# Kernel tuning notes

Measured on AMD Instinct MI355X. Metric: run time of the kernel, lower is better.

The kernel has to match this reference:

```python
import jax, jax.numpy as jnp
import numpy as np

N_NODES, N_EDGES, N_FEAT = 50000, 500000, 128
HID, LAT, N_GRAPHS = 256, 64, 512
HEADS, DH = 8, 32  # GAT: 8 heads x 32 = 256
EPS = 1e-5


def _seg_softmax(logits, seg, num):
    m = jax.ops.segment_max(logits, seg, num_segments=num)
    m = jnp.where(jnp.isfinite(m), m, 0.0)
    e = jnp.exp(logits - m[seg])
    s = jax.ops.segment_sum(e, seg, num_segments=num)
    return e / jnp.maximum(s[seg], 1e-16)


def _bn(h, g, b):  # BatchNorm1d, batch statistics
    mu = h.mean(0)
    var = h.var(0)
    return (h - mu) * jax.lax.rsqrt(var + EPS) * g + b


def _ln(h, g, b):
    mu = h.mean(-1, keepdims=True)
    var = h.var(-1, keepdims=True)
    return (h - mu) * jax.lax.rsqrt(var + EPS) * g + b


def setup_inputs() -> dict:
    key = jax.random.key(0)
    ks = iter(jax.random.split(key, 40))
    f = lambda *s: jax.random.normal(next(ks), s, dtype=jnp.float32) * 0.05
    inp = {
        'x': jax.random.normal(next(ks), (N_NODES, N_FEAT), dtype=jnp.float32),
        'W_emb': f(N_FEAT, HID), 'b_emb': f(HID),
        'W_gcn': f(HID, HID), 'b_gcn': f(HID),
        'W_gat': f(HID, HID), 'a_src': f(HEADS, DH), 'a_dst': f(HEADS, DH), 'b_gat': f(HID),
        'W_l': f(HID, HID), 'b_l': f(HID), 'W_r': f(HID, HID),
        'bn_gamma': jnp.ones((3, HID), jnp.float32), 'bn_beta': jnp.zeros((3, HID), jnp.float32),
        'Wg1': f(HID, HID // 2), 'bg1': f(HID // 2), 'Wg2': f(HID // 2, 1), 'bg2': f(1),
        'Wm1': f(HID, HID), 'bm1': f(HID), 'ln_m_g': jnp.ones(HID, jnp.float32), 'ln_m_b': jnp.zeros(HID, jnp.float32),
        'Wm2': f(HID, LAT), 'bm2': f(LAT),
        'Wv1': f(HID, HID), 'bv1': f(HID), 'ln_v_g': jnp.ones(HID, jnp.float32), 'ln_v_b': jnp.zeros(HID, jnp.float32),
        'Wv2': f(HID, LAT), 'bv2': f(LAT),
        'edge_index': jax.random.randint(next(ks), (2, N_EDGES), 0, N_NODES, dtype=jnp.int64),
        'batch': jnp.sort(jax.random.randint(next(ks), (N_NODES,), 0, N_GRAPHS, dtype=jnp.int64)),
    }
    return inp


def _forward(x, W_emb, b_emb, W_gcn, b_gcn, W_gat, a_src, a_dst, b_gat,
             W_l, b_l, W_r, bn_gamma, bn_beta, Wg1, bg1, Wg2, bg2,
             Wm1, bm1, ln_m_g, ln_m_b, Wm2, bm2, Wv1, bv1, ln_v_g, ln_v_b, Wv2, bv2,
             edge_index, batch):
    N = x.shape[0]
    loops = jnp.arange(N)
    src_sl = jnp.concatenate([edge_index[0], loops])  # with self-loops (GCN/GAT)
    dst_sl = jnp.concatenate([edge_index[1], loops])

    h = x @ W_emb + b_emb  # [N, HID]

    # --- layer 0: GCNConv ---
    deg = jax.ops.segment_sum(jnp.ones_like(dst_sl, dtype=h.dtype), dst_sl, num_segments=N)
    dis = jax.lax.rsqrt(deg)
    norm = dis[src_sl] * dis[dst_sl]  # [E+N]
    xt = h @ W_gcn
    out = jax.ops.segment_sum(xt[src_sl] * norm[:, None], dst_sl, num_segments=N) + b_gcn
    out = jax.nn.relu(_bn(out, bn_gamma[0], bn_beta[0]))
    h = h + out

    # --- layer 1: GATConv (8 heads, concat) ---
    xt = (h @ W_gat).reshape(N, HEADS, DH)
    al_src = (xt * a_src).sum(-1)  # [N, H]
    al_dst = (xt * a_dst).sum(-1)
    logits = jax.nn.leaky_relu(al_src[src_sl] + al_dst[dst_sl], 0.2)  # [E+N, H]
    alpha = _seg_softmax(logits, dst_sl, N)
    out = jax.ops.segment_sum(xt[src_sl] * alpha[:, :, None], dst_sl, num_segments=N)
    out = out.reshape(N, HID) + b_gat
    out = jax.nn.relu(_bn(out, bn_gamma[1], bn_beta[1]))
    h = h + out

    # --- layer 2: SAGEConv (mean aggregation, no self-loops) ---
    src, dst = edge_index[0], edge_index[1]
    cnt = jax.ops.segment_sum(jnp.ones_like(dst, dtype=h.dtype), dst, num_segments=N)
    nb_mean = jax.ops.segment_sum(h[src], dst, num_segments=N) / jnp.maximum(cnt, 1.0)[:, None]
    out = nb_mean @ W_l + b_l + h @ W_r
    out = jax.nn.relu(_bn(out, bn_gamma[2], bn_beta[2]))
    h = h + out

    # --- GlobalAttention pooling ---
    gate = (jax.nn.relu(h @ Wg1 + bg1) @ Wg2 + bg2)[:, 0]  # [N]
    w = _seg_softmax(gate, batch, N_GRAPHS)
    h_graph = jax.ops.segment_sum(h * w[:, None], batch, num_segments=N_GRAPHS)  # [G, HID]

    mu = jax.nn.relu(_ln(h_graph @ Wm1 + bm1, ln_m_g, ln_m_b)) @ Wm2 + bm2
    logvar = jax.nn.relu(_ln(h_graph @ Wv1 + bv1, ln_v_g, ln_v_b)) @ Wv2 + bv2
    return mu, logvar


def reference(x, W_emb, b_emb, W_gcn, b_gcn, W_gat, a_src, a_dst, b_gat,
              W_l, b_l, W_r, bn_gamma, bn_beta, Wg1, bg1, Wg2, bg2,
              Wm1, bm1, ln_m_g, ln_m_b, Wm2, bm2, Wv1, bv1, ln_v_g, ln_v_b, Wv2, bv2,
              edge_index, batch):
    return _forward(x, W_emb, b_emb, W_gcn, b_gcn, W_gat, a_src, a_dst, b_gat,
                    W_l, b_l, W_r, bn_gamma, bn_beta, Wg1, bg1, Wg2, bg2,
                    Wm1, bm1, ln_m_g, ln_m_b, Wm2, bm2, Wv1, bv1, ln_v_g, ln_v_b, Wv2, bv2,
                    edge_index, batch)
```

## Files before the change

### kernel.cpp

```cpp
#include <hip/hip_runtime.h>
#include <cstdint>
#include <cstddef>

#define N_NODES 50000
#define N_EDGES 500000
#define NG 512
#define HID 256
#define EPS 1e-5f
#define SCB 49

typedef __attribute__((ext_vector_type(8))) __bf16 bf16x8;
typedef __attribute__((ext_vector_type(8))) ushort u16x8;
typedef __attribute__((ext_vector_type(4))) float f32x4;

__device__ __forceinline__ ushort f2bf(float f) {
  uint32_t u = __float_as_uint(f);
  uint32_t r = (u + 0x7fffu + ((u >> 16) & 1u)) >> 16;
  return (ushort)r;
}
__device__ __forceinline__ float bfu(ushort u) { return __uint_as_float(((uint32_t)u) << 16); }
__device__ __forceinline__ float4 bf4(ushort4 u) {
  return make_float4(bfu(u.x), bfu(u.y), bfu(u.z), bfu(u.w));
}

__global__ void k_csr_count(const int* __restrict__ ei, int* __restrict__ cnt) {
  int e = blockIdx.x * 256 + threadIdx.x;
  if (e < N_EDGES) atomicAdd(&cnt[ei[N_EDGES + e]], 1);
}

__global__ void k_scan_part(const int* __restrict__ cnt, int* __restrict__ psum) {
  __shared__ int red[256];
  int tid = threadIdx.x;
  int i0 = blockIdx.x * 1024 + tid * 4;
  int s = 0;
  if (i0 + 4 <= N_NODES) {
    int4 v = *reinterpret_cast<const int4*>(cnt + i0);
    s = v.x + v.y + v.z + v.w;
  } else {
    for (int k = 0; k < 4; k++)
      if (i0 + k < N_NODES) s += cnt[i0 + k];
  }
  red[tid] = s;
  __syncthreads();
  for (int o = 128; o > 0; o >>= 1) {
    if (tid < o) red[tid] += red[tid + o];
    __syncthreads();
  }
  if (tid == 0) psum[blockIdx.x] = red[0];
}

__global__ void k_scan_top(const int* __restrict__ psum, int* __restrict__ boff,
                           int* __restrict__ row_ptr) {
  int t = threadIdx.x;
  int v = (t < SCB) ? psum[t] : 0;
  int own = v;
  for (int o = 1; o < 64; o <<= 1) {
    int u = __shfl_up(v, o);
    if (t >= o) v += u;
  }
  if (t < SCB) boff[t] = v - own;
  if (t == 63) row_ptr[N_NODES] = v;
}

__global__ void k_scan_out(const int* __restrict__ cnt, const int* __restrict__ boff,
                           int* __restrict__ row_ptr, float* __restrict__ dis) {
  __shared__ int ps[256];
  int tid = threadIdx.x;
  int i0 = blockIdx.x * 1024 + tid * 4;
  int v[4];
#pragma unroll
  for (int k = 0; k < 4; k++) v[k] = (i0 + k < N_NODES) ? cnt[i0 + k] : 0;
  int s = v[0] + v[1] + v[2] + v[3];
  ps[tid] = s;
  __syncthreads();
  for (int o = 1; o < 256; o <<= 1) {
    int add = (tid >= o) ? ps[tid - o] : 0;
    __syncthreads();
    ps[tid] += add;
    __syncthreads();
  }
  int run = boff[blockIdx.x] + ((tid > 0) ? ps[tid - 1] : 0);
#pragma unroll
  for (int k = 0; k < 4; k++) {
    if (i0 + k < N_NODES) {
      row_ptr[i0 + k] = run;
      dis[i0 + k] = rsqrtf((float)v[k] + 1.0f);
      run += v[k];
    }
  }
}

__global__ void k_csr_fill(const int* __restrict__ ei, const int* __restrict__ row_ptr,
                           int* __restrict__ fill, int* __restrict__ col_src) {
  int e = blockIdx.x * 256 + threadIdx.x;
  if (e >= N_EDGES) return;
  int s = ei[e], d = ei[N_EDGES + e];
  int pos = row_ptr[d] + atomicAdd(&fill[d], 1);
  col_src[pos] = s;
}

struct WtArgs {
  const float* src[6];
  ushort* dst[6];
  int K[6];
  int C[6];
  int off[6];
};

__global__ void k_wt_all(WtArgs a) {
  int b = blockIdx.x;
  int ji = 0;
#pragma unroll
  for (int t = 1; t < 6; t++)
    if (b >= a.off[t]) ji = t;
  int K = a.K[ji], C = a.C[ji];
  int i = (b - a.off[ji]) * 256 + threadIdx.x;
  int c = i / K, k = i - c * K;
  a.dst[ji][i] = f2bf(a.src[ji][k * C + c]);
}

template <int K, int C, bool DUAL, bool AFP32, bool GATE>
__global__ __launch_bounds__(256) void k_mgemm(
    const void* __restrict__ A1v, const ushort* __restrict__ W1t,
    const ushort* __restrict__ A2, const ushort* __restrict__ W2t,
    const float* __restrict__ bias, ushort* __restrict__ out_bf,
    const float* __restrict__ gw, const float* __restrict__ gb,
    float* __restrict__ gate, int M, int relu) {
  constexpr int KS = K / 32;
  constexpr int CHK = K / 8;
  constexpr int NPAN = C / 64;
  constexpr int NISS = (64 * CHK) / 256;
  constexpr int NTOT = NPAN * (DUAL ? 2 : 1);
  constexpr int PELEM = 64 * K;
  __shared__ ushort wlds[2 * PELEM];
  const int tid = threadIdx.x;
  const int lane = tid & 63;
  const int wid = tid >> 6;
  const int r16 = lane & 15;
  const int kg = lane >> 4;
  const int rbase = blockIdx.x * 64 + wid * 16;

  int arow = rbase + r16;
  if (arow >= M) arow = M - 1;

  bf16x8 af[KS], af2[KS];
  if constexpr (AFP32) {
    const float* ap = (const float*)A1v + (size_t)arow * K + kg * 8;
#pragma unroll
    for (int ks = 0; ks < KS; ks++) {
      float4 lo = *reinterpret_cast<const float4*>(ap + ks * 32);
      float4 hi = *reinterpret_cast<const float4*>(ap + ks * 32 + 4);
      union { u16x8 u; bf16x8 b; } cv;
      cv.u = (u16x8){f2bf(lo.x), f2bf(lo.y), f2bf(lo.z), f2bf(lo.w),
                     f2bf(hi.x), f2bf(hi.y), f2bf(hi.z), f2bf(hi.w)};
      af[ks] = cv.b;
    }
  } else {
    const ushort* ap = (const ushort*)A1v + (size_t)arow * K + kg * 8;
#pragma unroll
    for (int ks = 0; ks < KS; ks++)
      af[ks] = *reinterpret_cast<const bf16x8*>(ap + ks * 32);
  }
  if constexpr (DUAL) {
    const ushort* ap = A2 + (size_t)arow * K + kg * 8;
#pragma unroll
    for (int ks = 0; ks < KS; ks++)
      af2[ks] = *reinterpret_cast<const bf16x8*>(ap + ks * 32);
  }

  float greg[4] = {0.f, 0.f, 0.f, 0.f};
  f32x4 acc[4];

#define STAGE_ASYNC(WSRC, PAN, BUF)                                            \
  {                                                                            \
    const ushort* base_ = (WSRC) + (size_t)((PAN) * 64) * K;                   \
    _Pragma("unroll") for (int j = 0; j < NISS; j++) {                         \
      int p_ = j * 256 + tid;                                                  \
      int c_ = p_ / CHK, jj_ = p_ % CHK;                                       \
      const ushort* g_ = base_ + c_ * K + (jj_ ^ (c_ & 7)) * 8;                \
      ushort* l_ = &wlds[(BUF) * PELEM + (j * 256 + wid * 64) * 8];            \
      __builtin_amdgcn_global_load_lds(                                        \
          (const __attribute__((address_space(1))) void*)(g_),                 \
          (__attribute__((address_space(3))) void*)(l_), 16, 0, 0);            \
    }                                                                          \
  }

#define COMPUTE(AF, BUF)                                                       \
  {                                                                            \
    const ushort* wb_ = &wlds[(BUF) * PELEM];                                  \
    _Pragma("unroll") for (int ct = 0; ct < 4; ct++) {                         \
      bf16x8 wf[KS];                                                           \
      int colr = ct * 16 + r16;                                                \
      _Pragma("unroll") for (int ks = 0; ks < KS; ks++) {                      \
        int slot = colr * CHK + ((ks * 4 + kg) ^ (r16 & 7));                   \
        wf[ks] = *reinterpret_cast<const bf16x8*>(&wb_[slot * 8]);             \
      }                                                                        \
      _Pragma("unroll") for (int ks = 0; ks < KS; ks++)                        \
        acc[ct] = __builtin_amdgcn_mfma_f32_16x16x32_bf16((AF)[ks], wf[ks],    \
                                                          acc[ct], 0, 0, 0);   \
    }                                                                          \
  }

  STAGE_ASYNC(W1t, 0, 0);
  __syncthreads();

#pragma unroll
  for (int q = 0; q < NTOT; q++) {
    const int pan = DUAL ? (q >> 1) : q;
    const int pass = DUAL ? (q & 1) : 0;
    const int cur = q & 1;
    const int c0 = pan * 64;
    if (pass == 0) {
#pragma unroll
      for (int ct = 0; ct < 4; ct++) acc[ct] = (f32x4){0.f, 0.f, 0.f, 0.f};
    }
    if (q + 1 < NTOT) {
      const int npan = DUAL ? ((q + 1) >> 1) : (q + 1);
      const ushort* Wq = (DUAL && ((q + 1) & 1)) ? W2t : W1t;
      STAGE_ASYNC(Wq, npan, cur ^ 1);
    }
    if (DUAL && pass) {
      COMPUTE(af2, cur);
    } else {
      COMPUTE(af, cur);
    }
    if (pass == (DUAL ? 1 : 0)) {
      if constexpr (GATE) {
#pragma unroll
        for (int ct = 0; ct < 4; ct++) {
          int col = c0 + ct * 16 + r16;
          float bv = bias[col];
          float wv = gw[col];
#pragma unroll
          for (int i = 0; i < 4; i++) {
            float v = fmaxf(acc[ct][i] + bv, 0.f);
            greg[i] = fmaf(v, wv, greg[i]);
          }
        }
      } else {
#pragma unroll
        for (int ct = 0; ct < 4; ct++) {
          int col = c0 + ct * 16 + r16;
          float bv = bias ? bias[col] : 0.f;
#pragma unroll
          for (int i = 0; i < 4; i++) {
            int row = rbase + kg * 4 + i;
            if (row < M) {
              float v = acc[ct][i] + bv;
              if (relu) v = fmaxf(v, 0.f);
              out_bf[(size_t)row * C + col] = f2bf(v);
            }
          }
        }
      }
    }
    __syncthreads();
  }

  if constexpr (GATE) {
#pragma unroll
    for (int i = 0; i < 4; i++) {
#pragma unroll
      for (int o = 1; o < 16; o <<= 1) greg[i] += __shfl_xor(greg[i], o);
    }
    if (r16 == 0) {
      float b0 = gb[0];
#pragma unroll
      for (int i = 0; i < 4; i++) {
        int row = rbase + kg * 4 + i;
        if (row < M) gate[row] = greg[i] + b0;
      }
    }
  }
#undef STAGE_ASYNC
#undef COMPUTE
}

__global__ void k_gcn_agg(const ushort* __restrict__ xt, const float* __restrict__ dis,
                          const int* __restrict__ row_ptr, const int* __restrict__ col_src,
                          const float* __restrict__ b_gcn, ushort* __restrict__ outb) {
  int node = blockIdx.x * 4 + (threadIdx.x >> 6);
  if (node >= N_NODES) return;
  int lane = threadIdx.x & 63;
  int half = lane >> 5;
  int c0 = (lane & 31) * 8;
  float di = dis[node];
  float acc[8];
#pragma unroll
  for (int j = 0; j < 8; j++) acc[j] = 0.f;
  int b = row_ptr[node], e = row_ptr[node + 1];
  int g0 = b;
  for (; g0 + 4 <= e; g0 += 4) {
    int i0 = g0 + half * 2;
    int s0 = col_src[i0], s1 = col_src[i0 + 1];
    float w0 = di * dis[s0], w1 = di * dis[s1];
    u16x8 u0 = *reinterpret_cast<const u16x8*>(xt + (size_t)s0 * HID + c0);
    u16x8 u1 = *reinterpret_cast<const u16x8*>(xt + (size_t)s1 * HID + c0);
#pragma unroll
    for (int j = 0; j < 8; j++) {
      acc[j] = fmaf(bfu(u0[j]), w0, acc[j]);
      acc[j] = fmaf(bfu(u1[j]), w1, acc[j]);
    }
  }
  {
    int i0 = g0 + half * 2;
    int s0 = 0, s1 = 0;
    float w0 = 0.f, w1 = 0.f;
    if (i0 < e) { s0 = col_src[i0]; w0 = di * dis[s0]; }
    if (i0 + 1 < e) { s1 = col_src[i0 + 1]; w1 = di * dis[s1]; }
    u16x8 u0 = *reinterpret_cast<const u16x8*>(xt + (size_t)s0 * HID + c0);
    u16x8 u1 = *reinterpret_cast<const u16x8*>(xt + (size_t)s1 * HID + c0);
#pragma unroll
    for (int j = 0; j < 8; j++) {
      acc[j] = fmaf(bfu(u0[j]), w0, acc[j]);
      acc[j] = fmaf(bfu(u1[j]), w1, acc[j]);
    }
  }
#pragma unroll
  for (int j = 0; j < 8; j++) acc[j] += __shfl_xor(acc[j], 32);
  if (!half) {
    u16x8 un = *reinterpret_cast<const u16x8*>(xt + (size_t)node * HID + c0);
    float w0 = di * di;
    u16x8 r;
#pragma unroll
    for (int j = 0; j < 8; j++) {
      float v = fmaf(bfu(un[j]), w0, acc[j]) + b_gcn[c0 + j];
      r[j] = f2bf(v);
    }
    *reinterpret_cast<u16x8*>(outb + (size_t)node * HID + c0) = r;
  }
}

__global__ void k_gat_al(const ushort* __restrict__ xt, const float* __restrict__ a_src,
                         const float* __restrict__ a_dst, float* __restrict__ alsrc,
                         float* __restrict__ aldst) {
  int node = blockIdx.x * 4 + (threadIdx.x >> 6);
  if (node >= N_NODES) return;
  int lane = threadIdx.x & 63;
  float4 v = bf4(*reinterpret_cast<const ushort4*>(xt + (size_t)node * HID + lane * 4));
  float4 as = *reinterpret_cast<const float4*>(a_src + lane * 4);
  float4 ad = *reinterpret_cast<const float4*>(a_dst + lane * 4);
  float ps = v.x * as.x + v.y * as.y + v.z * as.z + v.w * as.w;
  float pd = v.x * ad.x + v.y * ad.y + v.z * ad.z + v.w * ad.w;
  for (int o = 1; o < 8; o <<= 1) { ps += __shfl_xor(ps, o); pd += __shfl_xor(pd, o); }
  if ((lane & 7) == 0) {
    alsrc[node * 8 + (lane >> 3)] = ps;
    aldst[node * 8 + (lane >> 3)] = pd;
  }
}

__device__ __forceinline__ float leaky02(float x) { return x > 0.f ? x : 0.2f * x; }

__global__ void k_gat_agg(const ushort* __restrict__ xt, const float* __restrict__ alsrc,
                          const float* __restrict__ aldst, const int* __restrict__ row_ptr,
                          const int* __restrict__ col_src, const float* __restrict__ b_gat,
                          ushort* __restrict__ outb) {
  int node = blockIdx.x * 4 + (threadIdx.x >> 6);
  if (node >= N_NODES) return;
  int lane = threadIdx.x & 63;
  int half = lane >> 5;
  int l32 = lane & 31;
  int c0 = l32 * 8;
  int hh = l32 >> 2;
  float ad = aldst[node * 8 + hh];
  float acc[8];
#pragma unroll
  for (int j = 0; j < 8; j++) acc[j] = 0.f;
  float s = 0.f;
  int b = row_ptr[node], e = row_ptr[node + 1];
  int g0 = b;
  for (; g0 + 4 <= e; g0 += 4) {
    int i0 = g0 + half * 2;
    int s0 = col_src[i0], s1 = col_src[i0 + 1];
    float a0 = __expf(leaky02(alsrc[s0 * 8 + hh] + ad));
    float a1 = __expf(leaky02(alsrc[s1 * 8 + hh] + ad));
    u16x8 u0 = *reinterpret_cast<const u16x8*>(xt + (size_t)s0 * HID + c0);
    u16x8 u1 = *reinterpret_cast<const u16x8*>(xt + (size_t)s1 * HID + c0);
    s += a0 + a1;
#pragma unroll
    for (int j = 0; j < 8; j++) {
      acc[j] = fmaf(bfu(u0[j]), a0, acc[j]);
      acc[j] = fmaf(bfu(u1[j]), a1, acc[j]);
    }
  }
  {
    int i0 = g0 + half * 2;
    int s0 = 0, s1 = 0;
    float a0 = 0.f, a1 = 0.f;
    if (i0 < e) { s0 = col_src[i0]; a0 = __expf(leaky02(alsrc[s0 * 8 + hh] + ad)); }
    if (i0 + 1 < e) { s1 = col_src[i0 + 1]; a1 = __expf(leaky02(alsrc[s1 * 8 + hh] + ad)); }
    u16x8 u0 = *reinterpret_cast<const u16x8*>(xt + (size_t)s0 * HID + c0);
    u16x8 u1 = *reinterpret_cast<const u16x8*>(xt + (size_t)s1 * HID + c0);
    s += a0 + a1;
#pragma unroll
    for (int j = 0; j < 8; j++) {
      acc[j] = fmaf(bfu(u0[j]), a0, acc[j]);
      acc[j] = fmaf(bfu(u1[j]), a1, acc[j]);
    }
  }
#pragma unroll
  for (int j = 0; j < 8; j++) acc[j] += __shfl_xor(acc[j], 32);
  s += __shfl_xor(s, 32);
  if (!half) {
    float e0 = __expf(leaky02(alsrc[node * 8 + hh] + ad));
    u16x8 un = *reinterpret_cast<const u16x8*>(xt + (size_t)node * HID + c0);
    float inv_s = 1.0f / (s + e0);
    u16x8 r;
#pragma unroll
    for (int j = 0; j < 8; j++) {
      float v = fmaf(bfu(un[j]), e0, acc[j]) * inv_s + b_gat[c0 + j];
      r[j] = f2bf(v);
    }
    *reinterpret_cast<u16x8*>(outb + (size_t)node * HID + c0) = r;
  }
}

__global__ void k_sage_agg(const ushort* __restrict__ h, const int* __restrict__ row_ptr,
                           const int* __restrict__ col_src, ushort* __restrict__ outb) {
  int node = blockIdx.x * 4 + (threadIdx.x >> 6);
  if (node >= N_NODES) return;
  int lane = threadIdx.x & 63;
  int half = lane >> 5;
  int c0 = (lane & 31) * 8;
  float acc[8];
#pragma unroll
  for (int j = 0; j < 8; j++) acc[j] = 0.f;
  int b = row_ptr[node], e = row_ptr[node + 1];
  int g0 = b;
  for (; g0 + 4 <= e; g0 += 4) {
    int i0 = g0 + half * 2;
    int s0 = col_src[i0], s1 = col_src[i0 + 1];
    u16x8 u0 = *reinterpret_cast<const u16x8*>(h + (size_t)s0 * HID + c0);
    u16x8 u1 = *reinterpret_cast<const u16x8*>(h + (size_t)s1 * HID + c0);
#pragma unroll
    for (int j = 0; j < 8; j++) acc[j] += bfu(u0[j]) + bfu(u1[j]);
  }
  {
    int i0 = g0 + half * 2;
    int s0 = 0, s1 = 0;
    float w0 = 0.f, w1 = 0.f;
    if (i0 < e) { s0 = col_src[i0]; w0 = 1.f; }
    if (i0 + 1 < e) { s1 = col_src[i0 + 1]; w1 = 1.f; }
    u16x8 u0 = *reinterpret_cast<const u16x8*>(h + (size_t)s0 * HID + c0);
    u16x8 u1 = *reinterpret_cast<const u16x8*>(h + (size_t)s1 * HID + c0);
#pragma unroll
    for (int j = 0; j < 8; j++) {
      acc[j] = fmaf(bfu(u0[j]), w0, acc[j]);
      acc[j] = fmaf(bfu(u1[j]), w1, acc[j]);
    }
  }
#pragma unroll
  for (int j = 0; j < 8; j++) acc[j] += __shfl_xor(acc[j], 32);
  if (!half) {
    float inv = 1.0f / fmaxf((float)(e - b), 1.0f);
    u16x8 r;
#pragma unroll
    for (int j = 0; j < 8; j++) r[j] = f2bf(acc[j] * inv);
    *reinterpret_cast<u16x8*>(outb + (size_t)node * HID + c0) = r;
  }
}

__global__ void k_bn_stats(const ushort* __restrict__ x, float* __restrict__ stats) {
  int c = threadIdx.x;
  float s = 0.f, q = 0.f;
  for (int r = blockIdx.x; r < N_NODES; r += gridDim.x) {
    float v = bfu(x[(size_t)r * HID + c]);
    s += v;
    q = fmaf(v, v, q);
  }
  atomicAdd(&stats[c], s);
  atomicAdd(&stats[HID + c], q);
}

__global__ void k_bn_apply(const ushort* __restrict__ x, const float* __restrict__ stats,
                           const float* __restrict__ gamma, const float* __restrict__ beta,
                           ushort* __restrict__ h_bf) {
  const float invN = 1.0f / (float)N_NODES;
  int total = N_NODES * 64;
  for (int i = blockIdx.x * 256 + threadIdx.x; i < total; i += gridDim.x * 256) {
    int c4 = (i & 63) * 4;
    float4 xv = bf4(*reinterpret_cast<const ushort4*>(x + (size_t)i * 4));
    float4 sm = *reinterpret_cast<const float4*>(stats + c4);
    float4 sq = *reinterpret_cast<const float4*>(stats + HID + c4);
    float4 gm = *reinterpret_cast<const float4*>(gamma + c4);
    float4 bt = *reinterpret_cast<const float4*>(beta + c4);
    float4 hv = bf4(*reinterpret_cast<const ushort4*>(h_bf + (size_t)i * 4));
#define BN1(f)                                                    \
  {                                                               \
    float mu = sm.f * invN;                                       \
    float var = sq.f * invN - mu * mu;                            \
    float sc = gm.f * rsqrtf(var + EPS);                          \
    float v = (xv.f - mu) * sc + bt.f;                            \
    hv.f += fmaxf(v, 0.f);                                        \
  }
    BN1(x) BN1(y) BN1(z) BN1(w)
#undef BN1
    *reinterpret_cast<ushort4*>(h_bf + (size_t)i * 4) =
        make_ushort4(f2bf(hv.x), f2bf(hv.y), f2bf(hv.z), f2bf(hv.w));
  }
}

__global__ void k_gstart(const int* __restrict__ batch, int* __restrict__ gstart) {
  int g = blockIdx.x * 256 + threadIdx.x;
  if (g > NG) return;
  int lo = 0, hi = N_NODES;
  while (lo < hi) {
    int mid = (lo + hi) >> 1;
    if (batch[mid] < g) lo = mid + 1; else hi = mid;
  }
  gstart[g] = lo;
}

__global__ void k_pool(const ushort* __restrict__ hb, const float* __restrict__ gate,
                       const int* __restrict__ gstart, float* __restrict__ hg) {
  __shared__ float red[256];
  __shared__ float wbuf[256];
  int g = blockIdx.x, tid = threadIdx.x;
  int b = gstart[g], e = gstart[g + 1];
  float m = -1e30f;
  for (int r = b + tid; r < e; r += 256) m = fmaxf(m, gate[r]);
  red[tid] = m;
  __syncthreads();
  for (int o = 128; o > 0; o >>= 1) {
    if (tid < o) red[tid] = fmaxf(red[tid], red[tid + o]);
    __syncthreads();
  }
  m = red[0];
  __syncthreads();
  float s = 0.f;
  for (int r = b + tid; r < e; r += 256) s += __expf(gate[r] - m);
  red[tid] = s;
  __syncthreads();
  for (int o = 128; o > 0; o >>= 1) {
    if (tid < o) red[tid] += red[tid + o];
    __syncthreads();
  }
  float inv = 1.0f / fmaxf(red[0], 1e-16f);
  __syncthreads();
  float acc = 0.f;
  for (int cb = b; cb < e; cb += 256) {
    int r = cb + tid;
    wbuf[tid] = (r < e) ? __expf(gate[r] - m) : 0.f;
    __syncthreads();
    int n = min(256, e - cb);
    for (int j = 0; j < n; j++)
      acc = fmaf(bfu(hb[(size_t)(cb + j) * HID + tid]), wbuf[j], acc);
    __syncthreads();
  }
  hg[(size_t)g * HID + tid] = acc * inv;
}

__global__ void k_mlp(const float* __restrict__ hg, const float* __restrict__ W1,
                      const float* __restrict__ b1, const float* __restrict__ lng,
                      const float* __restrict__ lnb, const float* __restrict__ W2,
                      const float* __restrict__ b2, float* __restrict__ out) {
  __shared__ float row[HID];
  __shared__ float z[HID];
  __shared__ float red[HID];
  int g = blockIdx.x, tid = threadIdx.x;
  row[tid] = hg[(size_t)g * HID + tid];
  __syncthreads();
  float acc = b1[tid];
  for (int k = 0; k < HID; k++) acc = fmaf(row[k], W1[(size_t)k * HID + tid], acc);
  red[tid] = acc;
  __syncthreads();
  for (int o = 128; o > 0; o >>= 1) {
    if (tid < o) red[tid] += red[tid + o];
    __syncthreads();
  }
  float mu = red[0] * (1.0f / HID);
  __syncthreads();
  red[tid] = acc * acc;
  __syncthreads();
  for (int o = 128; o > 0; o >>= 1) {
    if (tid < o) red[tid] += red[tid + o];
    __syncthreads();
  }
  float var = red[0] * (1.0f / HID) - mu * mu;
  float zz = (acc - mu) * rsqrtf(var + EPS) * lng[tid] + lnb[tid];
  z[tid] = fmaxf(zz, 0.f);
  __syncthreads();
  if (tid < 64) {
    float o = b2[tid];
    for (int k = 0; k < HID; k++) o = fmaf(z[k], W2[(size_t)k * 64 + tid], o);
    out[(size_t)g * 64 + tid] = o;
  }
}

extern "C" void kernel_launch(void* const* d_in, const int* in_sizes, int n_in,
                              void* d_out, int out_size, void* d_ws, size_t ws_size,
                              hipStream_t stream) {
  const float* x     = (const float*)d_in[0];
  const float* W_emb = (const float*)d_in[1];
  const float* b_emb = (const float*)d_in[2];
  const float* W_gcn = (const float*)d_in[3];
  const float* b_gcn = (const float*)d_in[4];
  const float* W_gat = (const float*)d_in[5];
  const float* a_src = (const float*)d_in[6];
  const float* a_dst = (const float*)d_in[7];
  const float* b_gat = (const float*)d_in[8];
  const float* W_l   = (const float*)d_in[9];
  const float* b_l   = (const float*)d_in[10];
  const float* W_r   = (const float*)d_in[11];
  const float* bn_g  = (const float*)d_in[12];
  const float* bn_b  = (const float*)d_in[13];
  const float* Wg1   = (const float*)d_in[14];
  const float* bg1   = (const float*)d_in[15];
  const float* Wg2   = (const float*)d_in[16];
  const float* bg2   = (const float*)d_in[17];
  const float* Wm1   = (const float*)d_in[18];
  const float* bm1   = (const float*)d_in[19];
  const float* lnmg  = (const float*)d_in[20];
  const float* lnmb  = (const float*)d_in[21];
  const float* Wm2   = (const float*)d_in[22];
  const float* bm2   = (const float*)d_in[23];
  const float* Wv1   = (const float*)d_in[24];
  const float* bv1   = (const float*)d_in[25];
  const float* lnvg  = (const float*)d_in[26];
  const float* lnvb  = (const float*)d_in[27];
  const float* Wv2   = (const float*)d_in[28];
  const float* bv2   = (const float*)d_in[29];
  const int* ei      = (const int*)d_in[30];
  const int* batch   = (const int*)d_in[31];
  float* out = (float*)d_out;

  float* ws = (float*)d_ws;
  float* h     = ws;
  float* t1    = h + (size_t)N_NODES * HID;
  float* alsrc = t1 + (size_t)N_NODES * HID;
  float* aldst = alsrc + N_NODES * 8;
  float* dis   = aldst + N_NODES * 8;
  float* gate  = dis + N_NODES;
  float* hg    = gate + N_NODES;
  float* zbase = hg + NG * HID;
  float* bnst  = zbase;
  int* row_cnt = (int*)(zbase + 3 * 512);
  int* fill    = row_cnt + N_NODES;
  int* row_ptr = fill + N_NODES;
  int* col_src = row_ptr + N_NODES + 1;
  int* gstart  = col_src + N_EDGES;
  int* psum    = gstart + NG + 1;
  int* boff    = psum + 64;

  ushort* t1b = (ushort*)t1;

  size_t off = (size_t)((char*)(boff + 64) - (char*)d_ws);
  off = (off + 15) & ~(size_t)15;
  ushort* h_bf   = (ushort*)((char*)d_ws + off);
  ushort* t0_bf  = h_bf + (size_t)N_NODES * HID;
  ushort* wemb_t = t0_bf + (size_t)N_NODES * HID;
  ushort* wgcn_t = wemb_t + 128 * 256;
  ushort* wgat_t = wgcn_t + 256 * 256;
  ushort* wr_t   = wgat_t + 256 * 256;
  ushort* wl_t   = wr_t + 256 * 256;
  ushort* wg1_t  = wl_t + 256 * 256;

  size_t zbytes = (size_t)3 * 512 * 4 + 2 * (size_t)N_NODES * 4;
  hipMemsetAsync(zbase, 0, zbytes, stream);

  k_csr_count<<<(N_EDGES + 255) / 256, 256, 0, stream>>>(ei, row_cnt);
  k_scan_part<<<SCB, 256, 0, stream>>>(row_cnt, psum);
  k_scan_top<<<1, 64, 0, stream>>>(psum, boff, row_ptr);
  k_scan_out<<<SCB, 256, 0, stream>>>(row_cnt, boff, row_ptr, dis);
  k_csr_fill<<<(N_EDGES + 255) / 256, 256, 0, stream>>>(ei, row_ptr, fill, col_src);

  WtArgs wa;
  wa.src[0] = W_emb; wa.dst[0] = wemb_t; wa.K[0] = 128; wa.C[0] = 256; wa.off[0] = 0;
  wa.src[1] = W_gcn; wa.dst[1] = wgcn_t; wa.K[1] = 256; wa.C[1] = 256; wa.off[1] = 128;
  wa.src[2] = W_gat; wa.dst[2] = wgat_t; wa.K[2] = 256; wa.C[2] = 256; wa.off[2] = 384;
  wa.src[3] = W_r;   wa.dst[3] = wr_t;   wa.K[3] = 256; wa.C[3] = 256; wa.off[3] = 640;
  wa.src[4] = W_l;   wa.dst[4] = wl_t;   wa.K[4] = 256; wa.C[4] = 256; wa.off[4] = 896;
  wa.src[5] = Wg1;   wa.dst[5] = wg1_t;  wa.K[5] = 256; wa.C[5] = 128; wa.off[5] = 1152;
  k_wt_all<<<1280, 256, 0, stream>>>(wa);

  const int RB = (N_NODES + 63) / 64;
  const int AB = (N_NODES + 3) / 4;

  k_mgemm<128, 256, false, true, false><<<RB, 256, 0, stream>>>(
      x, wemb_t, nullptr, nullptr, b_emb, h_bf, nullptr, nullptr, nullptr, N_NODES, 0);

  k_mgemm<256, 256, false, false, false><<<RB, 256, 0, stream>>>(
      h_bf, wgcn_t, nullptr, nullptr, nullptr, t0_bf, nullptr, nullptr, nullptr, N_NODES, 0);
  k_gcn_agg<<<AB, 256, 0, stream>>>(t0_bf, dis, row_ptr, col_src, b_gcn, t1b);
  k_bn_stats<<<256, 256, 0, stream>>>(t1b, bnst);
  k_bn_apply<<<1024, 256, 0, stream>>>(t1b, bnst, bn_g, bn_b, h_bf);

  k_mgemm<256, 256, false, false, false><<<RB, 256, 0, stream>>>(
      h_bf, wgat_t, nullptr, nullptr, nullptr, t0_bf, nullptr, nullptr, nullptr, N_NODES, 0);
  k_gat_al<<<AB, 256, 0, stream>>>(t0_bf, a_src, a_dst, alsrc, aldst);
  k_gat_agg<<<AB, 256, 0, stream>>>(t0_bf, alsrc, aldst, row_ptr, col_src, b_gat, t1b);
  k_bn_stats<<<256, 256, 0, stream>>>(t1b, bnst + 512);
  k_bn_apply<<<1024, 256, 0, stream>>>(t1b, bnst + 512, bn_g + HID, bn_b + HID, h_bf);

  k_sage_agg<<<AB, 256, 0, stream>>>(h_bf, row_ptr, col_src, t0_bf);
  k_mgemm<256, 256, true, false, false><<<RB, 256, 0, stream>>>(
      h_bf, wr_t, t0_bf, wl_t, b_l, t1b, nullptr, nullptr, nullptr, N_NODES, 0);
  k_bn_stats<<<256, 256, 0, stream>>>(t1b, bnst + 1024);
  k_bn_apply<<<1024, 256, 0, stream>>>(t1b, bnst + 1024, bn_g + 2 * HID, bn_b + 2 * HID, h_bf);

  k_mgemm<256, 128, false, false, true><<<RB, 256, 0, stream>>>(
      h_bf, wg1_t, nullptr, nullptr, bg1, nullptr, Wg2, bg2, gate, N_NODES, 1);
  k_gstart<<<3, 256, 0, stream>>>(batch, gstart);
  k_pool<<<NG, 256, 0, stream>>>(h_bf, gate, gstart, hg);

  k_mlp<<<NG, 256, 0, stream>>>(hg, Wm1, bm1, lnmg, lnmb, Wm2, bm2, out);
  k_mlp<<<NG, 256, 0, stream>>>(hg, Wv1, bv1, lnvg, lnvb, Wv2, bv2, out + (size_t)NG * 64);
}
```

Baseline: 614.8 us.

## Fuse GAT attention logits into GEMM, widen GEMM blocks, unroll gather loops

Folds the GAT per-head source and destination attention dot products into the GEMM epilogue through a GATAL template flag and deletes the separate k_gat_al kernel, which removes one launch and one full re-read of the projected features. The GEMM goes from 256 to 512 threads and 128 rows per block, so each staged weight panel is shared by twice as many rows, at the cost of fewer blocks and more LDS pressure per CU. The GCN, GAT and SAGE aggregation kernels get an 8-edge unrolled loop that keeps more independent gathers in flight, at the cost of higher register use.

```diff
diff --git a/kernel.cpp b/kernel.cpp
--- a/kernel.cpp
+++ b/kernel.cpp
@@ -119,17 +119,19 @@
   a.dst[ji][i] = f2bf(a.src[ji][k * C + c]);
 }
 
-template <int K, int C, bool DUAL, bool AFP32, bool GATE>
-__global__ __launch_bounds__(256) void k_mgemm(
+template <int K, int C, bool DUAL, bool AFP32, bool GATE, bool GATAL>
+__global__ __launch_bounds__(512) void k_mgemm(
     const void* __restrict__ A1v, const ushort* __restrict__ W1t,
     const ushort* __restrict__ A2, const ushort* __restrict__ W2t,
     const float* __restrict__ bias, ushort* __restrict__ out_bf,
     const float* __restrict__ gw, const float* __restrict__ gb,
-    float* __restrict__ gate, int M, int relu) {
+    float* __restrict__ gate, const float* __restrict__ asv,
+    const float* __restrict__ adv, float* __restrict__ als,
+    float* __restrict__ ald, int M, int relu) {
   constexpr int KS = K / 32;
   constexpr int CHK = K / 8;
   constexpr int NPAN = C / 64;
-  constexpr int NISS = (64 * CHK) / 256;
+  constexpr int NISS = (64 * CHK) / 512;
   constexpr int NTOT = NPAN * (DUAL ? 2 : 1);
   constexpr int PELEM = 64 * K;
   __shared__ ushort wlds[2 * PELEM];
@@ -138,7 +140,7 @@
   const int wid = tid >> 6;
   const int r16 = lane & 15;
   const int kg = lane >> 4;
-  const int rbase = blockIdx.x * 64 + wid * 16;
+  const int rbase = blockIdx.x * 128 + wid * 16;
 
   int arow = rbase + r16;
   if (arow >= M) arow = M - 1;
@@ -175,10 +177,10 @@
   {                                                                            \
     const ushort* base_ = (WSRC) + (size_t)((PAN) * 64) * K;                   \
     _Pragma("unroll") for (int j = 0; j < NISS; j++) {                         \
-      int p_ = j * 256 + tid;                                                  \
+      int p_ = j * 512 + tid;                                                  \
       int c_ = p_ / CHK, jj_ = p_ % CHK;                                       \
       const ushort* g_ = base_ + c_ * K + (jj_ ^ (c_ & 7)) * 8;                \
-      ushort* l_ = &wlds[(BUF) * PELEM + (j * 256 + wid * 64) * 8];            \
+      ushort* l_ = &wlds[(BUF) * PELEM + (j * 512 + wid * 64) * 8];            \
       __builtin_amdgcn_global_load_lds(                                        \
           (const __attribute__((address_space(1))) void*)(g_),                 \
           (__attribute__((address_space(3))) void*)(l_), 16, 0, 0);            \
@@ -253,6 +255,46 @@
           }
         }
       }
+      if constexpr (GATAL) {
+        float ps_[2][4], pd_[2][4];
+#pragma unroll
+        for (int h2 = 0; h2 < 2; h2++)
+#pragma unroll
+          for (int i = 0; i < 4; i++) { ps_[h2][i] = 0.f; pd_[h2][i] = 0.f; }
+#pragma unroll
+        for (int ct = 0; ct < 4; ct++) {
+          int col = c0 + ct * 16 + r16;
+          float as_ = asv[col], ad_ = adv[col];
+          int h2 = ct >> 1;
+#pragma unroll
+          for (int i = 0; i < 4; i++) {
+            ps_[h2][i] = fmaf(acc[ct][i], as_, ps_[h2][i]);
+            pd_[h2][i] = fmaf(acc[ct][i], ad_, pd_[h2][i]);
+          }
+        }
+#pragma unroll
+        for (int h2 = 0; h2 < 2; h2++)
+#pragma unroll
+          for (int i = 0; i < 4; i++) {
+#pragma unroll
+            for (int o = 1; o < 16; o <<= 1) {
+              ps_[h2][i] += __shfl_xor(ps_[h2][i], o);
+              pd_[h2][i] += __shfl_xor(pd_[h2][i], o);
+            }
+          }
+        if (r16 == 0) {
+#pragma unroll
+          for (int i = 0; i < 4; i++) {
+            int row = rbase + kg * 4 + i;
+            if (row < M) {
+              als[row * 8 + pan * 2 + 0] = ps_[0][i];
+              ald[row * 8 + pan * 2 + 0] = pd_[0][i];
+              als[row * 8 + pan * 2 + 1] = ps_[1][i];
+              ald[row * 8 + pan * 2 + 1] = pd_[1][i];
+            }
+          }
+        }
+      }
     }
     __syncthreads();
   }
@@ -290,6 +332,22 @@
   for (int j = 0; j < 8; j++) acc[j] = 0.f;
   int b = row_ptr[node], e = row_ptr[node + 1];
   int g0 = b;
+  for (; g0 + 8 <= e; g0 += 8) {
+    int i0 = g0 + half * 4;
+    int s0 = col_src[i0], s1 = col_src[i0 + 1], s2 = col_src[i0 + 2], s3 = col_src[i0 + 3];
+    float w0 = di * dis[s0], w1 = di * dis[s1], w2 = di * dis[s2], w3 = di * dis[s3];
+    u16x8 u0 = *reinterpret_cast<const u16x8*>(xt + (size_t)s0 * HID + c0);
+    u16x8 u1 = *reinterpret_cast<const u16x8*>(xt + (size_t)s1 * HID + c0);
+    u16x8 u2 = *reinterpret_cast<const u16x8*>(xt + (size_t)s2 * HID + c0);
+    u16x8 u3 = *reinterpret_cast<const u16x8*>(xt + (size_t)s3 * HID + c0);
+#pragma unroll
+    for (int j = 0; j < 8; j++) {
+      acc[j] = fmaf(bfu(u0[j]), w0, acc[j]);
+      acc[j] = fmaf(bfu(u1[j]), w1, acc[j]);
+      acc[j] = fmaf(bfu(u2[j]), w2, acc[j]);
+      acc[j] = fmaf(bfu(u3[j]), w3, acc[j]);
+    }
+  }
   for (; g0 + 4 <= e; g0 += 4) {
     int i0 = g0 + half * 2;
     int s0 = col_src[i0], s1 = col_src[i0 + 1];
@@ -328,24 +386,6 @@
       r[j] = f2bf(v);
     }
     *reinterpret_cast<u16x8*>(outb + (size_t)node * HID + c0) = r;
-  }
-}
-
-__global__ void k_gat_al(const ushort* __restrict__ xt, const float* __restrict__ a_src,
-                         const float* __restrict__ a_dst, float* __restrict__ alsrc,
-                         float* __restrict__ aldst) {
-  int node = blockIdx.x * 4 + (threadIdx.x >> 6);
-  if (node >= N_NODES) return;
-  int lane = threadIdx.x & 63;
-  float4 v = bf4(*reinterpret_cast<const ushort4*>(xt + (size_t)node * HID + lane * 4));
-  float4 as = *reinterpret_cast<const float4*>(a_src + lane * 4);
-  float4 ad = *reinterpret_cast<const float4*>(a_dst + lane * 4);
-  float ps = v.x * as.x + v.y * as.y + v.z * as.z + v.w * as.w;
-  float pd = v.x * ad.x + v.y * ad.y + v.z * ad.z + v.w * ad.w;
-  for (int o = 1; o < 8; o <<= 1) { ps += __shfl_xor(ps, o); pd += __shfl_xor(pd, o); }
-  if ((lane & 7) == 0) {
-    alsrc[node * 8 + (lane >> 3)] = ps;
-    aldst[node * 8 + (lane >> 3)] = pd;
   }
 }
 
@@ -369,6 +409,28 @@
   float s = 0.f;
   int b = row_ptr[node], e = row_ptr[node + 1];
   int g0 = b;
+  for (; g0 + 8 <= e; g0 += 8) {
+    int i0 = g0 + half * 4;
+    int s0 = col_src[i0], s1 = col_src[i0 + 1], s2 = col_src[i0 + 2], s3 = col_src[i0 + 3];
+    float g0v = alsrc[s0 * 8 + hh], g1v = alsrc[s1 * 8 + hh];
+    float g2v = alsrc[s2 * 8 + hh], g3v = alsrc[s3 * 8 + hh];
+    u16x8 u0 = *reinterpret_cast<const u16x8*>(xt + (size_t)s0 * HID + c0);
+    u16x8 u1 = *reinterpret_cast<const u16x8*>(xt + (size_t)s1 * HID + c0);
+    u16x8 u2 = *reinterpret_cast<const u16x8*>(xt + (size_t)s2 * HID + c0);
+    u16x8 u3 = *reinterpret_cast<const u16x8*>(xt + (size_t)s3 * HID + c0);
+    float a0 = __expf(leaky02(g0v + ad));
+    float a1 = __expf(leaky02(g1v + ad));
+    float a2 = __expf(leaky02(g2v + ad));
+    float a3 = __expf(leaky02(g3v + ad));
+    s += a0 + a1 + a2 + a3;
+#pragma unroll
+    for (int j = 0; j < 8; j++) {
+      acc[j] = fmaf(bfu(u0[j]), a0, acc[j]);
+      acc[j] = fmaf(bfu(u1[j]), a1, acc[j]);
+      acc[j] = fmaf(bfu(u2[j]), a2, acc[j]);
+      acc[j] = fmaf(bfu(u3[j]), a3, acc[j]);
+    }
+  }
   for (; g0 + 4 <= e; g0 += 4) {
     int i0 = g0 + half * 2;
     int s0 = col_src[i0], s1 = col_src[i0 + 1];
@@ -427,6 +489,17 @@
   for (int j = 0; j < 8; j++) acc[j] = 0.f;
   int b = row_ptr[node], e = row_ptr[node + 1];
   int g0 = b;
+  for (; g0 + 8 <= e; g0 += 8) {
+    int i0 = g0 + half * 4;
+    int s0 = col_src[i0], s1 = col_src[i0 + 1], s2 = col_src[i0 + 2], s3 = col_src[i0 + 3];
+    u16x8 u0 = *reinterpret_cast<const u16x8*>(h + (size_t)s0 * HID + c0);
+    u16x8 u1 = *reinterpret_cast<const u16x8*>(h + (size_t)s1 * HID + c0);
+    u16x8 u2 = *reinterpret_cast<const u16x8*>(h + (size_t)s2 * HID + c0);
+    u16x8 u3 = *reinterpret_cast<const u16x8*>(h + (size_t)s3 * HID + c0);
+#pragma unroll
+    for (int j = 0; j < 8; j++)
+      acc[j] += (bfu(u0[j]) + bfu(u1[j])) + (bfu(u2[j]) + bfu(u3[j]));
+  }
   for (; g0 + 4 <= e; g0 += 4) {
     int i0 = g0 + half * 2;
     int s0 = col_src[i0], s1 = col_src[i0 + 1];
@@ -673,33 +746,37 @@
   wa.src[5] = Wg1;   wa.dst[5] = wg1_t;  wa.K[5] = 256; wa.C[5] = 128; wa.off[5] = 1152;
   k_wt_all<<<1280, 256, 0, stream>>>(wa);
 
-  const int RB = (N_NODES + 63) / 64;
+  const int RB = (N_NODES + 127) / 128;
   const int AB = (N_NODES + 3) / 4;
 
-  k_mgemm<128, 256, false, true, false><<<RB, 256, 0, stream>>>(
-      x, wemb_t, nullptr, nullptr, b_emb, h_bf, nullptr, nullptr, nullptr, N_NODES, 0);
-
-  k_mgemm<256, 256, false, false, false><<<RB, 256, 0, stream>>>(
-      h_bf, wgcn_t, nullptr, nullptr, nullptr, t0_bf, nullptr, nullptr, nullptr, N_NODES, 0);
+  k_mgemm<128, 256, false, true, false, false><<<RB, 512, 0, stream>>>(
+      x, wemb_t, nullptr, nullptr, b_emb, h_bf, nullptr, nullptr, nullptr,
+      nullptr, nullptr, nullptr, nullptr, N_NODES, 0);
+
+  k_mgemm<256, 256, false, false, false, false><<<RB, 512, 0, stream>>>(
+      h_bf, wgcn_t, nullptr, nullptr, nullptr, t0_bf, nullptr, nullptr, nullptr,
+      nullptr, nullptr, nullptr, nullptr, N_NODES, 0);
   k_gcn_agg<<<AB, 256, 0, stream>>>(t0_bf, dis, row_ptr, col_src, b_gcn, t1b);
   k_bn_stats<<<256, 256, 0, stream>>>(t1b, bnst);
   k_bn_apply<<<1024, 256, 0, stream>>>(t1b, bnst, bn_g, bn_b, h_bf);
 
-  k_mgemm<256, 256, false, false, false><<<RB, 256, 0, stream>>>(
-      h_bf, wgat_t, nullptr, nullptr, nullptr, t0_bf, nullptr, nullptr, nullptr, N_NODES, 0);
-  k_gat_al<<<AB, 256, 0, stream>>>(t0_bf, a_src, a_dst, alsrc, aldst);
+  k_mgemm<256, 256, false, false, false, true><<<RB, 512, 0, stream>>>(
+      h_bf, wgat_t, nullptr, nullptr, nullptr, t0_bf, nullptr, nullptr, nullptr,
+      a_src, a_dst, alsrc, aldst, N_NODES, 0);
   k_gat_agg<<<AB, 256, 0, stream>>>(t0_bf, alsrc, aldst, row_ptr, col_src, b_gat, t1b);
   k_bn_stats<<<256, 256, 0, stream>>>(t1b, bnst + 512);
   k_bn_apply<<<1024, 256, 0, stream>>>(t1b, bnst + 512, bn_g + HID, bn_b + HID, h_bf);
 
   k_sage_agg<<<AB, 256, 0, stream>>>(h_bf, row_ptr, col_src, t0_bf);
-  k_mgemm<256, 256, true, false, false><<<RB, 256, 0, stream>>>(
-      h_bf, wr_t, t0_bf, wl_t, b_l, t1b, nullptr, nullptr, nullptr, N_NODES, 0);
+  k_mgemm<256, 256, true, false, false, false><<<RB, 512, 0, stream>>>(
+      h_bf, wr_t, t0_bf, wl_t, b_l, t1b, nullptr, nullptr, nullptr,
+      nullptr, nullptr, nullptr, nullptr, N_NODES, 0);
   k_bn_stats<<<256, 256, 0, stream>>>(t1b, bnst + 1024);
   k_bn_apply<<<1024, 256, 0, stream>>>(t1b, bnst + 1024, bn_g + 2 * HID, bn_b + 2 * HID, h_bf);
 
-  k_mgemm<256, 128, false, false, true><<<RB, 256, 0, stream>>>(
-      h_bf, wg1_t, nullptr, nullptr, bg1, nullptr, Wg2, bg2, gate, N_NODES, 1);
+  k_mgemm<256, 128, false, false, true, false><<<RB, 512, 0, stream>>>(
+      h_bf, wg1_t, nullptr, nullptr, bg1, nullptr, Wg2, bg2, gate,
+      nullptr, nullptr, nullptr, nullptr, N_NODES, 1);
   k_gstart<<<3, 256, 0, stream>>>(batch, gstart);
   k_pool<<<NG, 256, 0, stream>>>(h_bf, gate, gstart, hg);
 
```

Result: no change. 604.5 us (-1.7%).
